# Performance work log

Hardware: AMD Instinct MI355X
Metric: run time of the kernel (lower is better)

The kernel has to match this reference:

```python
import jax, jax.numpy as jnp
import numpy as np

KH, KW = 3, 3
STRIDE = 1
PAD = 1


def setup_inputs() -> dict:
    key = jax.random.key(0)
    kf, ko, kw_ = jax.random.split(key, 3)
    B, C, H, W = 4, 128, 96, 320
    Cout = 128
    features = jax.random.normal(kf, (B, C, H, W), dtype=jnp.float32)
    # perspective offsets in the original are O(offset_2d / D_RATIO) = O(2)
    offsets = jax.random.normal(ko, (B, 2 * KH * KW, H, W), dtype=jnp.float32) * 2.0
    weight = jax.random.normal(kw_, (Cout, C, KH, KW), dtype=jnp.float32) * (1.0 / np.sqrt(C * KH * KW))
    return {"features": features, "offsets": offsets, "weight": weight}


def _bilinear_sample(img, py, px):
    """img: [C,H,W]; py, px: [K,Ho,Wo] float sampling locations.
    Zero padding outside the image (torchvision deform_conv2d semantics).
    Returns [C,K,Ho,Wo]."""
    C, H, W = img.shape
    y0 = jnp.floor(py)
    x0 = jnp.floor(px)
    y1 = y0 + 1.0
    x1 = x0 + 1.0
    wy1 = py - y0
    wy0 = 1.0 - wy1
    wx1 = px - x0
    wx0 = 1.0 - wx1

    def gather(yy, xx):
        valid = (yy >= 0) & (yy <= H - 1) & (xx >= 0) & (xx <= W - 1)
        yi = jnp.clip(yy, 0, H - 1).astype(jnp.int32)
        xi = jnp.clip(xx, 0, W - 1).astype(jnp.int32)
        v = img[:, yi, xi]  # [C,K,Ho,Wo]
        return v * valid[None].astype(img.dtype)

    return (gather(y0, x0) * (wy0 * wx0)[None]
            + gather(y0, x1) * (wy0 * wx1)[None]
            + gather(y1, x0) * (wy1 * wx0)[None]
            + gather(y1, x1) * (wy1 * wx1)[None])


def deform_conv2d(x, offset, weight, stride=STRIDE, pad=PAD):
    B, C, H, W = x.shape
    Cout, Cin, kh, kw = weight.shape
    Ho = (H + 2 * pad - kh) // stride + 1
    Wo = (W + 2 * pad - kw) // stride + 1
    K = kh * kw
    # torchvision layout: channel 2k = dy, channel 2k+1 = dx, taps row-major
    off = offset.reshape(B, K, 2, Ho, Wo)
    ky, kx = jnp.meshgrid(jnp.arange(kh), jnp.arange(kw), indexing='ij')
    ky = ky.reshape(-1).astype(x.dtype)  # [K]
    kx = kx.reshape(-1).astype(x.dtype)
    hy = (jnp.arange(Ho) * stride - pad).astype(x.dtype)  # [Ho]
    wx = (jnp.arange(Wo) * stride - pad).astype(x.dtype)  # [Wo]
    base_y = ky[:, None, None] + hy[None, :, None]  # [K,Ho,1]
    base_x = kx[:, None, None] + wx[None, None, :]  # [K,1,Wo]
    py = base_y[None] + off[:, :, 0]  # [B,K,Ho,Wo]
    px = base_x[None] + off[:, :, 1]
    sampled = jax.vmap(_bilinear_sample)(x, py, px)  # [B,C,K,Ho,Wo]
    out = jnp.einsum('ok,bkn->bon',
                     weight.reshape(Cout, Cin * K),
                     sampled.reshape(B, Cin * K, Ho * Wo))
    return out.reshape(B, Cout, Ho, Wo)


def reference(features, offsets, weight):
    return deform_conv2d(features, offsets, weight)
```

## Files before the change

kernel.cpp:

```cpp
#include <hip/hip_runtime.h>
#include <hip/hip_fp16.h>

#define IH   96
#define IW   320
#define NB   4
#define CIN  128
#define COUT 128
#define NKP  9
#define HW   (IH*IW)

typedef float    f32x4 __attribute__((ext_vector_type(4)));
typedef _Float16 f16x8 __attribute__((ext_vector_type(8)));
typedef unsigned u32x4 __attribute__((ext_vector_type(4)));

__global__ __launch_bounds__(256) void k_pre(const float* __restrict__ feat,
                                             const float* __restrict__ w,
                                             unsigned* __restrict__ nhwc,
                                             _Float16* __restrict__ wb) {
    __shared__ float tile[32][129];
    int bid = blockIdx.x;
    int tid = threadIdx.x;

    if (bid < 3840) {
        int xc = bid % 10;
        int by = bid / 10;
        int y = by % IH;
        int b = by / IH;
        int x0 = xc * 32;
        const float* src = feat + (size_t)b * CIN * HW + (size_t)y * IW + x0;
#pragma unroll
        for (int i = 0; i < 16; ++i) {
            int idx = tid + 256 * i;
            int c = idx >> 5, xl = idx & 31;
            tile[xl][c] = src[(size_t)c * HW + xl];
        }
        __syncthreads();
        unsigned* d = nhwc + ((size_t)(b * IH + y) * IW + x0) * 64;
#pragma unroll
        for (int i = 0; i < 8; ++i) {
            int idx = tid + 256 * i;
            int c2 = idx & 63, xl = idx >> 6;
            __half2 p;
            p.x = __float2half(tile[xl][2 * c2]);
            p.y = __float2half(tile[xl][2 * c2 + 1]);
            d[xl * 64 + c2] = *(unsigned*)&p;
        }
        return;
    }
    bid -= 3840;
    int d = bid * 256 + tid;
    int kp = d >> 14;
    int row = (d >> 7) & 127;
    int j = d & 127;
    int csrc = j ^ ((row & 7) << 3);
    wb[d] = (_Float16)w[(row * CIN + csrc) * NKP + kp];
}

__global__ __launch_bounds__(256, 2) void k_main(const float* __restrict__ off,
                                                 const char* __restrict__ fb,
                                                 const _Float16* __restrict__ wbuf,
                                                 float* __restrict__ out) {
    __shared__ _Float16 wlds[2][16384];

    const int tid  = threadIdx.x;
    const int lane = tid & 63;
    const int wv   = tid >> 6;
    const int posl = lane & 15;
    const int kg   = lane >> 4;

    const int bid = (blockIdx.x & 7) * 240 + (blockIdx.x >> 3);
    const int n0  = bid * 64;
    const int b   = n0 / HW;
    const int rem = n0 - b * HW;
    const int ho  = rem / IW;
    const int wox = rem - ho * IW + wv * 16 + posl;

    const float* offp = off + (size_t)b * 18 * HW + ho * IW + wox;
    const unsigned bkg = ((unsigned)(b * HW) << 8) + 16 * kg;

    const int xorv = (posl & 7) << 4;
    int aoff[4];
#pragma unroll
    for (int s = 0; s < 4; ++s)
        aoff[s] = posl * 256 + ((64 * s + 16 * kg) ^ xorv);

    const int stg = wv * 4096 + lane * 8;

    f32x4 acc[8];
#pragma unroll
    for (int m = 0; m < 8; ++m) acc[m] = (f32x4){0.f, 0.f, 0.f, 0.f};

    {
        const _Float16* src = wbuf + stg;
#pragma unroll
        for (int j = 0; j < 8; ++j) {
            f16x8 v = *(const f16x8*)(src + j * 512);
            *(f16x8*)(&wlds[0][stg + j * 512]) = v;
        }
    }
    __syncthreads();

    for (int kp = 0; kp < NKP; ++kp) {
        const char* wc = (const char*)&wlds[kp & 1][0];
        const bool more = (kp + 1 < NKP);

        f16x8 stgv[8];
        if (more) {
            const _Float16* src = wbuf + (kp + 1) * 16384 + stg;
#pragma unroll
            for (int j = 0; j < 8; ++j)
                stgv[j] = *(const f16x8*)(src + j * 512);
        }

        const int ky = kp / 3, kx = kp - 3 * (kp / 3);
        float dy = offp[(size_t)(2 * kp) * HW];
        float dx = offp[(size_t)(2 * kp + 1) * HW];
        float py = (float)(ho - 1 + ky) + dy;
        float px = (float)(wox - 1 + kx) + dx;
        float y0f = floorf(py), x0f = floorf(px);
        float wy1 = py - y0f, wx1 = px - x0f;
        float wy0 = 1.f - wy1, wx0 = 1.f - wx1;
        int y0 = (int)y0f, x0 = (int)x0f, y1 = y0 + 1, x1 = x0 + 1;
        wy0 = (y0 >= 0 && y0 < IH) ? wy0 : 0.f;
        wy1 = (y1 >= 0 && y1 < IH) ? wy1 : 0.f;
        wx0 = (x0 >= 0 && x0 < IW) ? wx0 : 0.f;
        wx1 = (x1 >= 0 && x1 < IW) ? wx1 : 0.f;
        int yr0 = min(max(y0, 0), IH - 1) * IW, yr1 = min(max(y1, 0), IH - 1) * IW;
        int xc0 = min(max(x0, 0), IW - 1), xc1 = min(max(x1, 0), IW - 1);
        unsigned a00 = bkg + ((unsigned)(yr0 + xc0) << 8);
        unsigned a01 = bkg + ((unsigned)(yr0 + xc1) << 8);
        unsigned a10 = bkg + ((unsigned)(yr1 + xc0) << 8);
        unsigned a11 = bkg + ((unsigned)(yr1 + xc1) << 8);
        __half2 W00 = __half2half2(__float2half(wy0 * wx0));
        __half2 W01 = __half2half2(__float2half(wy0 * wx1));
        __half2 W10 = __half2half2(__float2half(wy1 * wx0));
        __half2 W11 = __half2half2(__float2half(wy1 * wx1));

#pragma unroll
        for (int s = 0; s < 4; ++s) {
            u32x4 u00 = *(const u32x4*)(fb + (a00 + 64u * s));
            u32x4 u01 = *(const u32x4*)(fb + (a01 + 64u * s));
            u32x4 u10 = *(const u32x4*)(fb + (a10 + 64u * s));
            u32x4 u11 = *(const u32x4*)(fb + (a11 + 64u * s));
            u32x4 bfu;
#pragma unroll
            for (int jd = 0; jd < 4; ++jd) {
                unsigned c00 = u00[jd], c01 = u01[jd], c10 = u10[jd], c11 = u11[jd];
                __half2 r = __hmul2(W00, *(__half2*)&c00);
                r = __hfma2(W01, *(__half2*)&c01, r);
                r = __hfma2(W10, *(__half2*)&c10, r);
                r = __hfma2(W11, *(__half2*)&c11, r);
                bfu[jd] = *(unsigned*)&r;
            }
            f16x8 bf = *(f16x8*)&bfu;
#pragma unroll
            for (int m = 0; m < 8; ++m) {
                f16x8 am = *(const f16x8*)(wc + m * 4096 + aoff[s]);
                acc[m] = __builtin_amdgcn_mfma_f32_16x16x32_f16(am, bf, acc[m], 0, 0, 0);
            }
        }

        if (more) {
            _Float16* dst = &wlds[(kp + 1) & 1][stg];
#pragma unroll
            for (int j = 0; j < 8; ++j)
                *(f16x8*)(dst + j * 512) = stgv[j];
        }
        __syncthreads();
    }

    float* ob = out + ((size_t)b * COUT + 4 * kg) * HW + ho * IW + wox;
#pragma unroll
    for (int m = 0; m < 8; ++m)
#pragma unroll
        for (int r = 0; r < 4; ++r)
            ob[(size_t)(m * 16 + r) * HW] = acc[m][r];
}

extern "C" void kernel_launch(void* const* d_in, const int* in_sizes, int n_in,
                              void* d_out, int out_size, void* d_ws, size_t ws_size,
                              hipStream_t stream) {
    const float* features = (const float*)d_in[0];
    const float* offsets  = (const float*)d_in[1];
    const float* weight   = (const float*)d_in[2];
    float* out = (float*)d_out;

    unsigned*  nhwc = (unsigned*)d_ws;
    _Float16*  wbuf = (_Float16*)((char*)d_ws + (size_t)NB * HW * CIN * 2);

    hipLaunchKernelGGL(k_pre, dim3(4416), dim3(256), 0, stream,
                       features, weight, nhwc, wbuf);
    hipLaunchKernelGGL(k_main, dim3((NB * HW) / 64), dim3(256), 0, stream,
                       offsets, (const char*)nhwc, wbuf, out);
}
```

Before: 273.8 us.

## Single-buffer weight LDS via direct global-to-LDS loads and raise occupancy

The double-buffered weight tile in shared memory becomes a single 32KB buffer, filled with global_load_lds (direct global-to-LDS transfers) instead of register staging, and launch bounds rise from 2 to 4 blocks per CU. Offset values are prefetched one kernel tap ahead, and all 16 gather loads per tap are issued before any blending. The aim is more waves per CU to hide gather latency and fewer staging registers. In exchange, each tap now needs two block barriers and the weight load is no longer overlapped with compute, so waves stall on that load.

```diff
diff --git a/kernel.cpp b/kernel.cpp
--- a/kernel.cpp
+++ b/kernel.cpp
@@ -56,11 +56,11 @@
     wb[d] = (_Float16)w[(row * CIN + csrc) * NKP + kp];
 }
 
-__global__ __launch_bounds__(256, 2) void k_main(const float* __restrict__ off,
+__global__ __launch_bounds__(256, 4) void k_main(const float* __restrict__ off,
                                                  const char* __restrict__ fb,
                                                  const _Float16* __restrict__ wbuf,
                                                  float* __restrict__ out) {
-    __shared__ _Float16 wlds[2][16384];
+    __shared__ _Float16 wlds[16384];
 
     const int tid  = threadIdx.x;
     const int lane = tid & 63;
@@ -84,39 +84,35 @@
     for (int s = 0; s < 4; ++s)
         aoff[s] = posl * 256 + ((64 * s + 16 * kg) ^ xorv);
 
-    const int stg = wv * 4096 + lane * 8;
+    const char* gstage0 = (const char*)wbuf + (size_t)wv * 8192 + lane * 16;
 
     f32x4 acc[8];
 #pragma unroll
     for (int m = 0; m < 8; ++m) acc[m] = (f32x4){0.f, 0.f, 0.f, 0.f};
 
-    {
-        const _Float16* src = wbuf + stg;
-#pragma unroll
-        for (int j = 0; j < 8; ++j) {
-            f16x8 v = *(const f16x8*)(src + j * 512);
-            *(f16x8*)(&wlds[0][stg + j * 512]) = v;
-        }
+#pragma unroll
+    for (int j = 0; j < 8; ++j) {
+        __builtin_amdgcn_global_load_lds(
+            (const __attribute__((address_space(1))) unsigned*)(gstage0 + j * 1024),
+            (__attribute__((address_space(3))) unsigned*)((char*)wlds + wv * 8192 + j * 1024),
+            16, 0, 0);
     }
+    float dy_c = offp[0];
+    float dx_c = offp[HW];
     __syncthreads();
 
     for (int kp = 0; kp < NKP; ++kp) {
-        const char* wc = (const char*)&wlds[kp & 1][0];
         const bool more = (kp + 1 < NKP);
 
-        f16x8 stgv[8];
+        float dy_n = 0.f, dx_n = 0.f;
         if (more) {
-            const _Float16* src = wbuf + (kp + 1) * 16384 + stg;
-#pragma unroll
-            for (int j = 0; j < 8; ++j)
-                stgv[j] = *(const f16x8*)(src + j * 512);
+            dy_n = offp[(size_t)(2 * kp + 2) * HW];
+            dx_n = offp[(size_t)(2 * kp + 3) * HW];
         }
 
         const int ky = kp / 3, kx = kp - 3 * (kp / 3);
-        float dy = offp[(size_t)(2 * kp) * HW];
-        float dx = offp[(size_t)(2 * kp + 1) * HW];
-        float py = (float)(ho - 1 + ky) + dy;
-        float px = (float)(wox - 1 + kx) + dx;
+        float py = (float)(ho - 1 + ky) + dy_c;
+        float px = (float)(wox - 1 + kx) + dx_c;
         float y0f = floorf(py), x0f = floorf(px);
         float wy1 = py - y0f, wx1 = px - x0f;
         float wy0 = 1.f - wy1, wx0 = 1.f - wx1;
@@ -136,16 +132,21 @@
         __half2 W10 = __half2half2(__float2half(wy1 * wx0));
         __half2 W11 = __half2half2(__float2half(wy1 * wx1));
 
+        u32x4 g00[4], g01[4], g10[4], g11[4];
 #pragma unroll
         for (int s = 0; s < 4; ++s) {
-            u32x4 u00 = *(const u32x4*)(fb + (a00 + 64u * s));
-            u32x4 u01 = *(const u32x4*)(fb + (a01 + 64u * s));
-            u32x4 u10 = *(const u32x4*)(fb + (a10 + 64u * s));
-            u32x4 u11 = *(const u32x4*)(fb + (a11 + 64u * s));
+            g00[s] = *(const u32x4*)(fb + (a00 + 64u * s));
+            g01[s] = *(const u32x4*)(fb + (a01 + 64u * s));
+            g10[s] = *(const u32x4*)(fb + (a10 + 64u * s));
+            g11[s] = *(const u32x4*)(fb + (a11 + 64u * s));
+        }
+
+#pragma unroll
+        for (int s = 0; s < 4; ++s) {
             u32x4 bfu;
 #pragma unroll
             for (int jd = 0; jd < 4; ++jd) {
-                unsigned c00 = u00[jd], c01 = u01[jd], c10 = u10[jd], c11 = u11[jd];
+                unsigned c00 = g00[s][jd], c01 = g01[s][jd], c10 = g10[s][jd], c11 = g11[s][jd];
                 __half2 r = __hmul2(W00, *(__half2*)&c00);
                 r = __hfma2(W01, *(__half2*)&c01, r);
                 r = __hfma2(W10, *(__half2*)&c10, r);
@@ -155,18 +156,26 @@
             f16x8 bf = *(f16x8*)&bfu;
 #pragma unroll
             for (int m = 0; m < 8; ++m) {
-                f16x8 am = *(const f16x8*)(wc + m * 4096 + aoff[s]);
+                f16x8 am = *(const f16x8*)((const char*)wlds + m * 4096 + aoff[s]);
                 acc[m] = __builtin_amdgcn_mfma_f32_16x16x32_f16(am, bf, acc[m], 0, 0, 0);
             }
         }
 
+        dy_c = dy_n;
+        dx_c = dx_n;
+
         if (more) {
-            _Float16* dst = &wlds[(kp + 1) & 1][stg];
-#pragma unroll
-            for (int j = 0; j < 8; ++j)
-                *(f16x8*)(dst + j * 512) = stgv[j];
-        }
-        __syncthreads();
+            __syncthreads();
+            const char* gs = gstage0 + (size_t)(kp + 1) * 32768;
+#pragma unroll
+            for (int j = 0; j < 8; ++j) {
+                __builtin_amdgcn_global_load_lds(
+                    (const __attribute__((address_space(1))) unsigned*)(gs + j * 1024),
+                    (__attribute__((address_space(3))) unsigned*)((char*)wlds + wv * 8192 + j * 1024),
+                    16, 0, 0);
+            }
+            __syncthreads();
+        }
     }
 
     float* ob = out + ((size_t)b * COUT + 4 * kg) * HW + ho * IW + wox;
```

After: 269.3 us. About the same (-1.7%).
